# Performance work log

Hardware: AMD Instinct MI355X
Metric: run time of the kernel (lower is better)

Reference implementation:

```python
import jax, jax.numpy as jnp
import numpy as np

# ---- constants matching the original module's globals ----
H = 16          # self.h: number of bit levels; self.n = h per the source
TP = 8          # self.tp: parallel coordinate channels
N_K = 2         # random masks per flipped bit
T = 512         # T_train: tokens per block
N_TRNBR = 128   # neighbor count
K_VOCAB = 128   # sampled vocab count
N_VOCAB = 50257 # full vocab size V for sampled softmax correction
D = 256         # embedding dim
RATIO_COS = 1.0
RATIO_CRO = 0.1
C_CNC = 2 * H * N_K + 1  # candidate locations per token = 65


def setup_inputs() -> dict:
    key = jax.random.key(0)
    ks = jax.random.split(key, 8)
    n = H  # code: self.n = h
    sta_loc = jax.random.randint(ks[0], (T, TP), 1 - n, n, dtype=jnp.int32)
    nei_loc = jax.random.randint(ks[1], (T, N_TRNBR, TP), 1 - n, n, dtype=jnp.int32)
    voc_loc = jax.random.randint(ks[2], (T, K_VOCAB, TP), 1 - n, n, dtype=jnp.int32)
    sta_emb = jax.random.normal(ks[3], (T, D), dtype=jnp.float32)
    nei_emb = jax.random.normal(ks[4], (T, N_TRNBR, D), dtype=jnp.float32)
    voc_emb = jax.random.normal(ks[5], (T, K_VOCAB, D), dtype=jnp.float32)
    # raw random numbers for generate_random_masks: randint(0, self.n)
    rand_masks = jax.random.randint(ks[6], (T, H, N_K, TP), 0, n, dtype=jnp.int32)
    # converge mode: mask is all ones (generate_mask with converge=True)
    mask = jnp.ones((T, N_TRNBR), dtype=bool)
    return {"sta_loc": sta_loc, "nei_loc": nei_loc, "voc_loc": voc_loc,
            "sta_emb": sta_emb, "nei_emb": nei_emb, "voc_emb": voc_emb,
            "rand_masks": rand_masks, "mask": mask}


def _cos_similarity(c1, c2):
    # sign product: (+1 if >=0 else -1) for each operand
    sg = ((2 * (c1 >= 0).astype(jnp.int32) - 1) *
          (2 * (c2 >= 0).astype(jnp.int32) - 1)).astype(jnp.float32)
    x = ((jnp.abs(c1) ^ jnp.abs(c2)) + 1).astype(jnp.float32)
    # torch.frexp exponent of v>=1 equals floor(log2(v)) + 1
    expo = jnp.floor(jnp.log2(x)) + 1.0
    return sg * (1.0 - expo / H)


def _connection(sta_loc, rand_masks):
    bits = jnp.arange(H, dtype=jnp.int32)
    flip_masks = (1 << bits)                          # [H]
    flipped = sta_loc[:, None, :] ^ flip_masks[None, :, None]  # [T,H,TP]
    # note operator precedence in source: rn & (2**i - 1)
    rm = rand_masks & (flip_masks - 1)[None, :, None, None]    # [T,H,N_K,TP]
    res = (flipped[:, :, None, :] ^ rm).reshape(sta_loc.shape[0], H * N_K, TP)
    return jnp.concatenate([res, sta_loc[:, None, :], -res], axis=1)  # [T,C,TP]


def _normalize(x):
    return x / jnp.maximum(jnp.linalg.norm(x, axis=-1, keepdims=True), 1e-12)


def reference(sta_loc, nei_loc, voc_loc, sta_emb, nei_emb, voc_emb, rand_masks, mask):
    cnc_loc = _connection(sta_loc, rand_masks)          # [T, C, TP]
    lth = mask.sum(axis=1).astype(jnp.float32) + 1e-12  # [T]

    # euclidean-space cosine targets: [T, N_trnbr]
    eu_cos_val = jnp.einsum('td,tnd->tn', _normalize(sta_emb), _normalize(nei_emb))
    # use_eu_norm == True branch: ||sta|| * ||voc|| -> [T, K_vocab]
    eu_cro_nrm = (jnp.linalg.norm(sta_emb, axis=-1, keepdims=True) *
                  jnp.linalg.norm(voc_emb, axis=-1))

    pos_loc = jnp.concatenate([nei_loc, voc_loc], axis=1)           # [T, P, TP]
    cos_sta_pos = _cos_similarity(sta_loc[:, None, :], pos_loc)     # [T, P, TP]
    cos_sta_pos_sum = cos_sta_pos.sum(axis=-1)                      # [T, P]
    cos_cnc_pos = _cos_similarity(cnc_loc[:, None, :, :], pos_loc[:, :, None, :])  # [T,P,C,TP]
    ct_val = (cos_sta_pos_sum[:, :, None, None]
              - cos_sta_pos[:, :, None, :] + cos_cnc_pos) / TP      # [T,P,C,TP]

    # cosine-matching loss over neighbors
    eu = eu_cos_val[:, :, None, None]                               # [T,N,1,1]
    loss_cos = ((ct_val[:, :N_TRNBR] - eu) ** 2 * jnp.abs(eu)
                * mask[:, :, None, None].astype(jnp.float32))
    loss_cos = loss_cos.sum(axis=1) / lth[:, None, None]            # [T, C, TP]

    # sampled softmax CE (uniform proposal), positive class at vocab index 0
    z = ct_val[:, N_TRNBR:] * eu_cro_nrm[:, :, None, None]          # [T, K, C, TP]
    corr = jnp.where(jnp.arange(K_VOCAB) == 0, 0.0,
                     jnp.log(N_VOCAB / K_VOCAB)).astype(jnp.float32)
    zc = z + corr[None, :, None, None]
    loss_cro = jax.scipy.special.logsumexp(zc, axis=1) - zc[:, 0]   # [T, C, TP]

    loss_tot = RATIO_COS * loss_cos + RATIO_CRO * loss_cro

    # get_best_loc with cur_portion=1.0, cur_tp=tp -> pure argmin selection
    idx = jnp.argmin(loss_tot, axis=1)                              # [T, TP]
    gather = lambda a: jnp.take_along_axis(a, idx[:, None, :], axis=1)[:, 0]
    selected_locs = gather(cnc_loc)                                 # [T, TP]
    real_loss_cos = gather(loss_cos).mean(axis=-1)                  # [T]
    real_loss_cro = gather(loss_cro).mean(axis=-1)
    real_loss_tot = gather(loss_tot).mean(axis=-1)
    return selected_locs, real_loss_cos, real_loss_cro, real_loss_tot
```

## Files before the change

kernel.cpp:

```cpp
#include <hip/hip_runtime.h>
#include <math.h>

#define T_DIM 512
#define TP 8
#define NC 65
#define NJ 128
#define BLOCK 576
#define LOG2E 1.4426950408889634f
#define LN2   0.6931471805599453f
#define CORR_L2 8.617045f

__device__ __forceinline__ float i2f(int x) { return __int_as_float(x); }
__device__ __forceinline__ int   f2i(float x) { return __float_as_int(x); }

__device__ __forceinline__ int cand_v(int c, int sta, const int* s_rand, int p) {
    if (c == 32) return sta;
    const int cc = (c < 32) ? c : (c - 33);
    const int h = cc >> 1;
    const int r = (sta ^ (1 << h)) ^ (s_rand[cc * TP + p] & ((1 << h) - 1));
    return (c < 32) ? r : -r;
}

#define COS_STEP(va, vs, X, acc) do {                                   \
    const int _x = (va) ^ (X).x;                                        \
    const float _u8 = fmaf((float)__clz(_x + 1), 0.0078125f, -0.125f);  \
    const float _d = i2f(f2i(_u8) ^ ((vs) ^ (X).y)) + i2f((X).z);       \
    (acc) = fmaf(_d * _d, i2f((X).w), (acc));                           \
} while (0)

#define CRO_Z(va, vs, X) ({                                             \
    const int _x = (va) ^ (X).x;                                        \
    const float _u0 = fmaf((float)__clz(_x + 1), 0.0625f, -1.0f);       \
    const float _u = i2f(f2i(_u0) ^ ((vs) ^ (X).y));                    \
    fmaf(_u, i2f((X).w), i2f((X).z));                                   \
})

__device__ __forceinline__ float cos_body1(int va, int vs, const int4* pc) {
    float a0 = 0.f, a1 = 0.f;
    #pragma unroll 2
    for (int j = 0; j < NJ; j += 2) {
        const int4 x = pc[j * 8];
        const int4 y = pc[(j + 1) * 8];
        COS_STEP(va, vs, x, a0);
        COS_STEP(va, vs, y, a1);
    }
    return (a0 + a1) * 0.0078125f;
}

__device__ __forceinline__ void cos_body2(int vaA, int vsA, int vaB, int vsB,
                                          const int4* pc, float* oA, float* oB) {
    float a0 = 0.f, a1 = 0.f, b0 = 0.f, b1 = 0.f;
    #pragma unroll 2
    for (int j = 0; j < NJ; j += 2) {
        const int4 x = pc[j * 8];
        const int4 y = pc[(j + 1) * 8];
        COS_STEP(vaA, vsA, x, a0);
        COS_STEP(vaB, vsB, x, b0);
        COS_STEP(vaA, vsA, y, a1);
        COS_STEP(vaB, vsB, y, b1);
    }
    *oA = (a0 + a1) * 0.0078125f;
    *oB = (b0 + b1) * 0.0078125f;
}

__device__ __forceinline__ float cro_body1(int va, int vs, const int4* pc, float M) {
    const int4 x0 = pc[0];
    const float z0 = CRO_Z(va, vs, x0) - M;
    float s0 = __builtin_amdgcn_exp2f(z0);
    const int4 x1 = pc[8];
    float s1 = __builtin_amdgcn_exp2f(CRO_Z(va, vs, x1) - M);
    #pragma unroll 2
    for (int k = 2; k < NJ; k += 2) {
        const int4 x = pc[k * 8];
        const int4 y = pc[(k + 1) * 8];
        s0 += __builtin_amdgcn_exp2f(CRO_Z(va, vs, x) - M);
        s1 += __builtin_amdgcn_exp2f(CRO_Z(va, vs, y) - M);
    }
    const float S = fmaxf(s0 + s1, 1e-38f);
    return (__builtin_amdgcn_logf(S) - z0) * LN2;
}

__device__ __forceinline__ void cro_body2(int vaA, int vsA, int vaB, int vsB,
                                          const int4* pc, float M, float* oA, float* oB) {
    const int4 x0 = pc[0];
    const float zA0 = CRO_Z(vaA, vsA, x0) - M;
    const float zB0 = CRO_Z(vaB, vsB, x0) - M;
    float sA0 = __builtin_amdgcn_exp2f(zA0);
    float sB0 = __builtin_amdgcn_exp2f(zB0);
    const int4 x1 = pc[8];
    float sA1 = __builtin_amdgcn_exp2f(CRO_Z(vaA, vsA, x1) - M);
    float sB1 = __builtin_amdgcn_exp2f(CRO_Z(vaB, vsB, x1) - M);
    #pragma unroll 2
    for (int k = 2; k < NJ; k += 2) {
        const int4 x = pc[k * 8];
        const int4 y = pc[(k + 1) * 8];
        sA0 += __builtin_amdgcn_exp2f(CRO_Z(vaA, vsA, x) - M);
        sB0 += __builtin_amdgcn_exp2f(CRO_Z(vaB, vsB, x) - M);
        sA1 += __builtin_amdgcn_exp2f(CRO_Z(vaA, vsA, y) - M);
        sB1 += __builtin_amdgcn_exp2f(CRO_Z(vaB, vsB, y) - M);
    }
    const float SA = fmaxf(sA0 + sA1, 1e-38f);
    const float SB = fmaxf(sB0 + sB1, 1e-38f);
    *oA = (__builtin_amdgcn_logf(SA) - zA0) * LN2;
    *oB = (__builtin_amdgcn_logf(SB) - zB0) * LN2;
}

__global__ __launch_bounds__(BLOCK, 5) void cg_fused(
    const int* __restrict__ sta_loc,
    const int* __restrict__ nei_loc,
    const int* __restrict__ voc_loc,
    const float* __restrict__ sta_emb,
    const float* __restrict__ nei_emb,
    const float* __restrict__ voc_emb,
    const int* __restrict__ rand_masks,
    float* __restrict__ out)
{
    const int t = blockIdx.x;
    const int tid = threadIdx.x;

    __shared__ int4  s_pc4[2][NJ * TP];
    __shared__ float s_cspT[2][TP * 132];
    __shared__ float s_css[2][NJ];
    __shared__ float s_w[2][NJ];
    __shared__ float s_dot[NJ];
    __shared__ float s_nn[2][NJ];
    __shared__ float s_lcos[NC * TP], s_lcro[NC * TP];
    __shared__ float s_Mpart[9 * 8];
    __shared__ float s_ss;
    __shared__ int   s_sta[TP];
    __shared__ int   s_rand[256];

    if (tid < 256) s_rand[tid] = rand_masks[t * 256 + tid];

    if (tid < 512) {
        const int g = tid >> 2, sub = tid & 3;
        const float4* sp = (const float4*)(sta_emb + (size_t)t * 256);
        const float4* np = (const float4*)(nei_emb + ((size_t)t * NJ + g) * 256);
        const float4* vp = (const float4*)(voc_emb + ((size_t)t * NJ + g) * 256);
        float dd = 0.f, nnn = 0.f, nnv = 0.f, ss = 0.f;
        #pragma unroll 4
        for (int i = 0; i < 16; ++i) {
            const int i4 = sub + 4 * i;
            const float4 a = sp[i4];
            const float4 b = np[i4];
            const float4 c = vp[i4];
            dd  += a.x * b.x + a.y * b.y + a.z * b.z + a.w * b.w;
            nnn += b.x * b.x + b.y * b.y + b.z * b.z + b.w * b.w;
            nnv += c.x * c.x + c.y * c.y + c.z * c.z + c.w * c.w;
            if (g == 0) ss += a.x * a.x + a.y * a.y + a.z * a.z + a.w * a.w;
        }
        dd  += __shfl_xor(dd, 1);  dd  += __shfl_xor(dd, 2);
        nnn += __shfl_xor(nnn, 1); nnn += __shfl_xor(nnn, 2);
        nnv += __shfl_xor(nnv, 1); nnv += __shfl_xor(nnv, 2);
        if (g == 0) { ss += __shfl_xor(ss, 1); ss += __shfl_xor(ss, 2); }
        if (sub == 0) {
            s_dot[g] = dd; s_nn[0][g] = nnn; s_nn[1][g] = nnv;
            if (g == 0) s_ss = ss;
        }
    } else {
        const int l = tid - 512;
        if (l < TP) s_sta[l] = sta_loc[t * TP + l];
        const int4 sta4 = ((const int4*)(sta_loc + t * TP))[l & 1];
        const int sarr[4] = {sta4.x, sta4.y, sta4.z, sta4.w};
        #pragma unroll
        for (int side = 0; side < 2; ++side) {
            const int* loc = side ? voc_loc : nei_loc;
            const int4* lp = (const int4*)(loc + (size_t)t * 1024);
            #pragma unroll
            for (int q = 0; q < 4; ++q) {
                const int4 pl4 = lp[q * 64 + l];
                const int j = q * 32 + (l >> 1);
                const int parr[4] = {pl4.x, pl4.y, pl4.z, pl4.w};
                #pragma unroll
                for (int e = 0; e < 4; ++e) {
                    const int pl = parr[e];
                    const int sta = sarr[e];
                    const int idx = q * 256 + 4 * l + e;
                    const int qa = pl < 0 ? -pl : pl;
                    const int qsgn = pl & 0x80000000;
                    const int sa = sta < 0 ? -sta : sta;
                    const int x = sa ^ qa;
                    const float u0 = fmaf((float)__clz(x + 1), 0.0625f, -1.0f);
                    const float csp = i2f(f2i(u0) ^ ((sta ^ pl) & 0x80000000));
                    ((int2*)&s_pc4[side][idx])[0] = make_int2(qa, qsgn);
                    s_cspT[side][(4 * (l & 1) + e) * 132 + j] = csp;
                }
            }
        }
    }
    __syncthreads();

    if (tid < 256) {
        const int j = tid >> 1, side = tid & 1;
        float cs = 0.f;
        #pragma unroll
        for (int p = 0; p < TP; ++p) cs += s_cspT[side][p * 132 + j];
        s_css[side][j] = cs;
        const float ns = sqrtf(s_ss);
        const float nn = s_nn[side][j];
        if (side == 0)
            s_w[0][j] = s_dot[j] / (fmaxf(sqrtf(nn), 1e-12f) * fmaxf(ns, 1e-12f));
        else
            s_w[1][j] = ns * sqrtf(nn) * (0.125f * LOG2E);
    }
    __syncthreads();

    {
        float mloc = -INFINITY;
        #pragma unroll
        for (int k = 0; k < 4; ++k) {
            const int item = tid + k * BLOCK;
            if (item < 2048) {
                const int side = item >> 10, idx = item & 1023;
                const int j = idx >> 3, p = idx & 7;
                const float csp = s_cspT[side][p * 132 + j];
                const float b = s_css[side][j] - csp;
                const float w = s_w[side][j];
                float z2, w2;
                if (side == 0) { z2 = fmaf(b, 0.125f, -w); w2 = fabsf(w); }
                else {
                    z2 = fmaf(b, w, j ? CORR_L2 : 0.0f);
                    w2 = w;
                    mloc = fmaxf(mloc, z2 + w);
                }
                ((int2*)&s_pc4[side][idx])[1] = make_int2(f2i(z2), f2i(w2));
            }
        }
        mloc = fmaxf(mloc, __shfl_xor(mloc, 8));
        mloc = fmaxf(mloc, __shfl_xor(mloc, 16));
        mloc = fmaxf(mloc, __shfl_xor(mloc, 32));
        const int lane = tid & 63;
        if (lane < 8) s_Mpart[(tid >> 6) * 8 + lane] = mloc;
    }
    __syncthreads();

    if (tid < 256) {
        const int gk = tid >> 3, p = tid & 7;
        const int sta = s_sta[p];
        const int vA = cand_v(2 * gk, sta, s_rand, p);
        const int vB = cand_v(2 * gk + 1, sta, s_rand, p);
        cos_body2(vA < 0 ? -vA : vA, vA & 0x80000000,
                  vB < 0 ? -vB : vB, vB & 0x80000000, s_pc4[0] + p,
                  &s_lcos[(2 * gk) * TP + p], &s_lcos[(2 * gk + 1) * TP + p]);
    } else if (tid < 512) {
        const int w = tid - 256, gk = w >> 3, p = w & 7;
        const int sta = s_sta[p];
        const int vA = cand_v(2 * gk, sta, s_rand, p);
        const int vB = cand_v(2 * gk + 1, sta, s_rand, p);
        float M = s_Mpart[p];
        #pragma unroll
        for (int wv = 1; wv < 9; ++wv) M = fmaxf(M, s_Mpart[wv * 8 + p]);
        cro_body2(vA < 0 ? -vA : vA, vA & 0x80000000,
                  vB < 0 ? -vB : vB, vB & 0x80000000, s_pc4[1] + p, M,
                  &s_lcro[(2 * gk) * TP + p], &s_lcro[(2 * gk + 1) * TP + p]);
    } else if (tid < 520) {
        const int p = tid - 512;
        const int v = cand_v(64, s_sta[p], s_rand, p);
        s_lcos[64 * TP + p] =
            cos_body1(v < 0 ? -v : v, v & 0x80000000, s_pc4[0] + p);
    } else if (tid < 528) {
        const int p = tid - 520;
        const int v = cand_v(64, s_sta[p], s_rand, p);
        float M = s_Mpart[p];
        #pragma unroll
        for (int wv = 1; wv < 9; ++wv) M = fmaxf(M, s_Mpart[wv * 8 + p]);
        s_lcro[64 * TP + p] =
            cro_body1(v < 0 ? -v : v, v & 0x80000000, s_pc4[1] + p, M);
    }
    __syncthreads();

    float vc = 0.f, vr = 0.f, vt = 0.f;
    if (tid < TP) {
        const int p = tid;
        float best = INFINITY, blc = 0.f, blr = 0.f;
        int bc = 0;
        for (int c = 0; c < NC; ++c) {
            const float lc = s_lcos[c * TP + p];
            const float lr = s_lcro[c * TP + p];
            const float lt = fmaf(0.1f, lr, lc);
            if (lt < best) { best = lt; bc = c; blc = lc; blr = lr; }
        }
        out[t * TP + p] = (float)cand_v(bc, s_sta[p], s_rand, p);
        vc = blc; vr = blr; vt = best;
    }
    if (tid < 64) {
        vc += __shfl_xor(vc, 1); vc += __shfl_xor(vc, 2); vc += __shfl_xor(vc, 4);
        vr += __shfl_xor(vr, 1); vr += __shfl_xor(vr, 2); vr += __shfl_xor(vr, 4);
        vt += __shfl_xor(vt, 1); vt += __shfl_xor(vt, 2); vt += __shfl_xor(vt, 4);
        if (tid == 0) {
            out[T_DIM * TP + t] = vc * 0.125f;
            out[T_DIM * TP + T_DIM + t] = vr * 0.125f;
            out[T_DIM * TP + 2 * T_DIM + t] = vt * 0.125f;
        }
    }
}

extern "C" void kernel_launch(void* const* d_in, const int* in_sizes, int n_in,
                              void* d_out, int out_size, void* d_ws, size_t ws_size,
                              hipStream_t stream) {
    const int* sta_loc = (const int*)d_in[0];
    const int* nei_loc = (const int*)d_in[1];
    const int* voc_loc = (const int*)d_in[2];
    const float* sta_emb = (const float*)d_in[3];
    const float* nei_emb = (const float*)d_in[4];
    const float* voc_emb = (const float*)d_in[5];
    const int* rand_masks = (const int*)d_in[6];
    float* out = (float*)d_out;

    cg_fused<<<T_DIM, BLOCK, 0, stream>>>(
        sta_loc, nei_loc, voc_loc, sta_emb, nei_emb, voc_emb, rand_masks, out);
}
```

Baseline: 197.9 us.

## Distribute candidate loss work across all waves with lane-split reductions

Replaces the per-thread full-neighbor loops (which used only 528 of 576 threads and left most waves idle) with round-robin tasks over 9 waves, each lane handling a slice of neighbors and reducing via shuffles. Also batches the embedding loads into groups of four before the arithmetic and raises the launch-bounds occupancy hint from 5 to 8. The tighter register budget risks spills, and the center candidate is computed redundantly in paired tasks.

```diff
diff --git a/kernel.cpp b/kernel.cpp
--- a/kernel.cpp
+++ b/kernel.cpp
@@ -35,77 +35,7 @@
     fmaf(_u, i2f((X).w), i2f((X).z));                                   \
 })
 
-__device__ __forceinline__ float cos_body1(int va, int vs, const int4* pc) {
-    float a0 = 0.f, a1 = 0.f;
-    #pragma unroll 2
-    for (int j = 0; j < NJ; j += 2) {
-        const int4 x = pc[j * 8];
-        const int4 y = pc[(j + 1) * 8];
-        COS_STEP(va, vs, x, a0);
-        COS_STEP(va, vs, y, a1);
-    }
-    return (a0 + a1) * 0.0078125f;
-}
-
-__device__ __forceinline__ void cos_body2(int vaA, int vsA, int vaB, int vsB,
-                                          const int4* pc, float* oA, float* oB) {
-    float a0 = 0.f, a1 = 0.f, b0 = 0.f, b1 = 0.f;
-    #pragma unroll 2
-    for (int j = 0; j < NJ; j += 2) {
-        const int4 x = pc[j * 8];
-        const int4 y = pc[(j + 1) * 8];
-        COS_STEP(vaA, vsA, x, a0);
-        COS_STEP(vaB, vsB, x, b0);
-        COS_STEP(vaA, vsA, y, a1);
-        COS_STEP(vaB, vsB, y, b1);
-    }
-    *oA = (a0 + a1) * 0.0078125f;
-    *oB = (b0 + b1) * 0.0078125f;
-}
-
-__device__ __forceinline__ float cro_body1(int va, int vs, const int4* pc, float M) {
-    const int4 x0 = pc[0];
-    const float z0 = CRO_Z(va, vs, x0) - M;
-    float s0 = __builtin_amdgcn_exp2f(z0);
-    const int4 x1 = pc[8];
-    float s1 = __builtin_amdgcn_exp2f(CRO_Z(va, vs, x1) - M);
-    #pragma unroll 2
-    for (int k = 2; k < NJ; k += 2) {
-        const int4 x = pc[k * 8];
-        const int4 y = pc[(k + 1) * 8];
-        s0 += __builtin_amdgcn_exp2f(CRO_Z(va, vs, x) - M);
-        s1 += __builtin_amdgcn_exp2f(CRO_Z(va, vs, y) - M);
-    }
-    const float S = fmaxf(s0 + s1, 1e-38f);
-    return (__builtin_amdgcn_logf(S) - z0) * LN2;
-}
-
-__device__ __forceinline__ void cro_body2(int vaA, int vsA, int vaB, int vsB,
-                                          const int4* pc, float M, float* oA, float* oB) {
-    const int4 x0 = pc[0];
-    const float zA0 = CRO_Z(vaA, vsA, x0) - M;
-    const float zB0 = CRO_Z(vaB, vsB, x0) - M;
-    float sA0 = __builtin_amdgcn_exp2f(zA0);
-    float sB0 = __builtin_amdgcn_exp2f(zB0);
-    const int4 x1 = pc[8];
-    float sA1 = __builtin_amdgcn_exp2f(CRO_Z(vaA, vsA, x1) - M);
-    float sB1 = __builtin_amdgcn_exp2f(CRO_Z(vaB, vsB, x1) - M);
-    #pragma unroll 2
-    for (int k = 2; k < NJ; k += 2) {
-        const int4 x = pc[k * 8];
-        const int4 y = pc[(k + 1) * 8];
-        sA0 += __builtin_amdgcn_exp2f(CRO_Z(vaA, vsA, x) - M);
-        sB0 += __builtin_amdgcn_exp2f(CRO_Z(vaB, vsB, x) - M);
-        sA1 += __builtin_amdgcn_exp2f(CRO_Z(vaA, vsA, y) - M);
-        sB1 += __builtin_amdgcn_exp2f(CRO_Z(vaB, vsB, y) - M);
-    }
-    const float SA = fmaxf(sA0 + sA1, 1e-38f);
-    const float SB = fmaxf(sB0 + sB1, 1e-38f);
-    *oA = (__builtin_amdgcn_logf(SA) - zA0) * LN2;
-    *oB = (__builtin_amdgcn_logf(SB) - zB0) * LN2;
-}
-
-__global__ __launch_bounds__(BLOCK, 5) void cg_fused(
+__global__ __launch_bounds__(BLOCK, 8) void cg_fused(
     const int* __restrict__ sta_loc,
     const int* __restrict__ nei_loc,
     const int* __restrict__ voc_loc,
@@ -138,16 +68,21 @@
         const float4* np = (const float4*)(nei_emb + ((size_t)t * NJ + g) * 256);
         const float4* vp = (const float4*)(voc_emb + ((size_t)t * NJ + g) * 256);
         float dd = 0.f, nnn = 0.f, nnv = 0.f, ss = 0.f;
-        #pragma unroll 4
-        for (int i = 0; i < 16; ++i) {
-            const int i4 = sub + 4 * i;
-            const float4 a = sp[i4];
-            const float4 b = np[i4];
-            const float4 c = vp[i4];
-            dd  += a.x * b.x + a.y * b.y + a.z * b.z + a.w * b.w;
-            nnn += b.x * b.x + b.y * b.y + b.z * b.z + b.w * b.w;
-            nnv += c.x * c.x + c.y * c.y + c.z * c.z + c.w * c.w;
-            if (g == 0) ss += a.x * a.x + a.y * a.y + a.z * a.z + a.w * a.w;
+        #pragma unroll
+        for (int q = 0; q < 4; ++q) {
+            float4 a[4], b[4], c[4];
+            #pragma unroll
+            for (int i = 0; i < 4; ++i) {
+                const int i4 = sub + 4 * (q * 4 + i);
+                a[i] = sp[i4]; b[i] = np[i4]; c[i] = vp[i4];
+            }
+            #pragma unroll
+            for (int i = 0; i < 4; ++i) {
+                dd  += a[i].x * b[i].x + a[i].y * b[i].y + a[i].z * b[i].z + a[i].w * b[i].w;
+                nnn += b[i].x * b[i].x + b[i].y * b[i].y + b[i].z * b[i].z + b[i].w * b[i].w;
+                nnv += c[i].x * c[i].x + c[i].y * c[i].y + c[i].z * c[i].z + c[i].w * c[i].w;
+                if (g == 0) ss += a[i].x * a[i].x + a[i].y * a[i].y + a[i].z * a[i].z + a[i].w * a[i].w;
+            }
         }
         dd  += __shfl_xor(dd, 1);  dd  += __shfl_xor(dd, 2);
         nnn += __shfl_xor(nnn, 1); nnn += __shfl_xor(nnn, 2);
@@ -234,38 +169,79 @@
     }
     __syncthreads();
 
-    if (tid < 256) {
-        const int gk = tid >> 3, p = tid & 7;
+    {
+        const int wv = tid >> 6, l = tid & 63;
+        const int p = l & 7;
         const int sta = s_sta[p];
-        const int vA = cand_v(2 * gk, sta, s_rand, p);
-        const int vB = cand_v(2 * gk + 1, sta, s_rand, p);
-        cos_body2(vA < 0 ? -vA : vA, vA & 0x80000000,
-                  vB < 0 ? -vB : vB, vB & 0x80000000, s_pc4[0] + p,
-                  &s_lcos[(2 * gk) * TP + p], &s_lcos[(2 * gk + 1) * TP + p]);
-    } else if (tid < 512) {
-        const int w = tid - 256, gk = w >> 3, p = w & 7;
-        const int sta = s_sta[p];
-        const int vA = cand_v(2 * gk, sta, s_rand, p);
-        const int vB = cand_v(2 * gk + 1, sta, s_rand, p);
         float M = s_Mpart[p];
         #pragma unroll
-        for (int wv = 1; wv < 9; ++wv) M = fmaxf(M, s_Mpart[wv * 8 + p]);
-        cro_body2(vA < 0 ? -vA : vA, vA & 0x80000000,
-                  vB < 0 ? -vB : vB, vB & 0x80000000, s_pc4[1] + p, M,
-                  &s_lcro[(2 * gk) * TP + p], &s_lcro[(2 * gk + 1) * TP + p]);
-    } else if (tid < 520) {
-        const int p = tid - 512;
-        const int v = cand_v(64, s_sta[p], s_rand, p);
-        s_lcos[64 * TP + p] =
-            cos_body1(v < 0 ? -v : v, v & 0x80000000, s_pc4[0] + p);
-    } else if (tid < 528) {
-        const int p = tid - 520;
-        const int v = cand_v(64, s_sta[p], s_rand, p);
-        float M = s_Mpart[p];
-        #pragma unroll
-        for (int wv = 1; wv < 9; ++wv) M = fmaxf(M, s_Mpart[wv * 8 + p]);
-        s_lcro[64 * TP + p] =
-            cro_body1(v < 0 ? -v : v, v & 0x80000000, s_pc4[1] + p, M);
+        for (int w8 = 1; w8 < 9; ++w8) M = fmaxf(M, s_Mpart[w8 * 8 + p]);
+
+        for (int tsk = wv; tsk < 66; tsk += 9) {
+            const int side = tsk & 1;
+            const int cp = tsk >> 1;
+            const int cA = (cp == 32) ? 64 : 2 * cp;
+            const int cB = (cp == 32) ? 64 : 2 * cp + 1;
+            const int vA = cand_v(cA, sta, s_rand, p);
+            const int vB = cand_v(cB, sta, s_rand, p);
+            const int vaA = vA < 0 ? -vA : vA, vsA = vA & 0x80000000;
+            const int vaB = vB < 0 ? -vB : vB, vsB = vB & 0x80000000;
+
+            if (side == 0) {
+                const int4* pcf = s_pc4[0];
+                float aA = 0.f, aB = 0.f;
+                #pragma unroll
+                for (int q = 0; q < 4; ++q) {
+                    const int4 x0 = pcf[q * 256 + l];
+                    const int4 x1 = pcf[q * 256 + 64 + l];
+                    const int4 x2 = pcf[q * 256 + 128 + l];
+                    const int4 x3 = pcf[q * 256 + 192 + l];
+                    COS_STEP(vaA, vsA, x0, aA); COS_STEP(vaB, vsB, x0, aB);
+                    COS_STEP(vaA, vsA, x1, aA); COS_STEP(vaB, vsB, x1, aB);
+                    COS_STEP(vaA, vsA, x2, aA); COS_STEP(vaB, vsB, x2, aB);
+                    COS_STEP(vaA, vsA, x3, aA); COS_STEP(vaB, vsB, x3, aB);
+                }
+                aA += __shfl_xor(aA, 8);  aB += __shfl_xor(aB, 8);
+                aA += __shfl_xor(aA, 16); aB += __shfl_xor(aB, 16);
+                aA += __shfl_xor(aA, 32); aB += __shfl_xor(aB, 32);
+                if (l < 8) {
+                    s_lcos[cA * TP + p] = aA * 0.0078125f;
+                    s_lcos[cB * TP + p] = aB * 0.0078125f;
+                }
+            } else {
+                const int4* pcf = s_pc4[1];
+                float sA = 0.f, sB = 0.f, z0A = 0.f, z0B = 0.f;
+                #pragma unroll
+                for (int q = 0; q < 4; ++q) {
+                    const int4 x0 = pcf[q * 256 + l];
+                    const int4 x1 = pcf[q * 256 + 64 + l];
+                    const int4 x2 = pcf[q * 256 + 128 + l];
+                    const int4 x3 = pcf[q * 256 + 192 + l];
+                    {
+                        const float zA = CRO_Z(vaA, vsA, x0) - M;
+                        const float zB = CRO_Z(vaB, vsB, x0) - M;
+                        if (q == 0) { z0A = zA; z0B = zB; }
+                        sA += __builtin_amdgcn_exp2f(zA);
+                        sB += __builtin_amdgcn_exp2f(zB);
+                    }
+                    sA += __builtin_amdgcn_exp2f(CRO_Z(vaA, vsA, x1) - M);
+                    sB += __builtin_amdgcn_exp2f(CRO_Z(vaB, vsB, x1) - M);
+                    sA += __builtin_amdgcn_exp2f(CRO_Z(vaA, vsA, x2) - M);
+                    sB += __builtin_amdgcn_exp2f(CRO_Z(vaB, vsB, x2) - M);
+                    sA += __builtin_amdgcn_exp2f(CRO_Z(vaA, vsA, x3) - M);
+                    sB += __builtin_amdgcn_exp2f(CRO_Z(vaB, vsB, x3) - M);
+                }
+                sA += __shfl_xor(sA, 8);  sB += __shfl_xor(sB, 8);
+                sA += __shfl_xor(sA, 16); sB += __shfl_xor(sB, 16);
+                sA += __shfl_xor(sA, 32); sB += __shfl_xor(sB, 32);
+                if (l < 8) {
+                    s_lcro[cA * TP + p] =
+                        (__builtin_amdgcn_logf(fmaxf(sA, 1e-38f)) - z0A) * LN2;
+                    s_lcro[cB * TP + p] =
+                        (__builtin_amdgcn_logf(fmaxf(sB, 1e-38f)) - z0B) * LN2;
+                }
+            }
+        }
     }
     __syncthreads();
 
```

After: 199.7 us. Within noise of the previous version (+0.9%).
